# Kernel tuning notes

Measured on AMD Instinct MI355X. Metric: run time of the kernel, lower is better.

## Reference

```python
import jax, jax.numpy as jnp
import numpy as np

N, E = 50000, 800000          # nodes, directed edges
DIN, DH, DOUT = 128, 256, 128  # feature dims


def setup_inputs() -> dict:
    key = jax.random.key(0)
    ks = jax.random.split(key, 8)
    glorot = lambda k, fin, fout: jax.random.normal(k, (fin, fout), jnp.float32) * np.float32(1.0 / np.sqrt(fin))
    x = jax.random.normal(ks[0], (N, DIN), jnp.float32)
    edge_index = jax.random.randint(ks[1], (2, E), 0, N, dtype=jnp.int64)
    return {
        "x": x,
        "edge_index": edge_index,
        "W1_l": glorot(ks[2], DIN, DH),   # applied to aggregated neighbors
        "b1": jnp.zeros((DH,), jnp.float32),
        "W1_r": glorot(ks[3], DIN, DH),   # root weight
        "W2_l": glorot(ks[4], DH, DOUT),
        "b2": jnp.zeros((DOUT,), jnp.float32),
        "W2_r": glorot(ks[5], DH, DOUT),
    }


def _sage_conv(x, src, dst, W_l, b, W_r):
    """PyG SAGEConv (mean aggr): lin_l(mean_j x_j) + lin_r(x_i)."""
    n = x.shape[0]
    agg = jax.ops.segment_sum(x[src], dst, num_segments=n)          # [N, D]
    deg = jax.ops.segment_sum(jnp.ones((src.shape[0], 1), x.dtype), dst, num_segments=n)
    agg = agg / jnp.maximum(deg, 1.0)                               # mean over in-neighbors
    return agg @ W_l + b + x @ W_r


def reference(x, edge_index, W1_l, b1, W1_r, W2_l, b2, W2_r):
    src, dst = edge_index[0], edge_index[1]
    h = jax.nn.relu(_sage_conv(x, src, dst, W1_l, b1, W1_r))
    return _sage_conv(h, src, dst, W2_l, b2, W2_r)
```

## Files before the change

### kernel.cpp

```cpp
#include <hip/hip_runtime.h>
#include <hip/hip_bf16.h>
#include <cstdint>


static inline size_t align_up(size_t x, size_t a) { return (x + a - 1) & ~(a - 1); }

using short8 = __attribute__((ext_vector_type(8))) short;
using f32x4  = __attribute__((ext_vector_type(4))) float;

#define BSHIFT 6
#define PB 98

__device__ __forceinline__ float bfpair_lo(unsigned int v) {
  union { unsigned int i; float f; } u; u.i = v << 16; return u.f;
}
__device__ __forceinline__ float bfpair_hi(unsigned int v) {
  union { unsigned int i; float f; } u; u.i = v & 0xffff0000u; return u.f;
}
__device__ __forceinline__ unsigned short f2bf(float f) {
  union { float f; unsigned int i; } u; u.f = f;
  unsigned int r = u.i + 0x7fffu + ((u.i >> 16) & 1u);
  return (unsigned short)(r >> 16);
}

__device__ __forceinline__ void gload_lds16(const void* g, void* l) {
  __builtin_amdgcn_global_load_lds(
      (const __attribute__((address_space(1))) void*)g,
      (__attribute__((address_space(3))) void*)l, 16, 0, 0);
}


__global__ __launch_bounds__(256) void bhist_kernel(const int* __restrict__ dst,
                                                    int* __restrict__ blockhist,
                                                    int E, int chunk) {
  __shared__ int h[1024];
  const int t = threadIdx.x;
  const int pb = blockIdx.x;
  #pragma unroll
  for (int i = t; i < 1024; i += 256) h[i] = 0;
  __syncthreads();
  const int e0 = pb * chunk;
  int e1 = e0 + chunk; if (e1 > E) e1 = E;
  for (int e = e0 + t; e < e1; e += 256) atomicAdd(&h[dst[e] >> BSHIFT], 1);
  __syncthreads();
  #pragma unroll
  for (int i = t; i < 1024; i += 256) blockhist[pb * 1024 + i] = h[i];
}

__global__ __launch_bounds__(256) void colscan_kernel(int* __restrict__ blockhist,
                                                      int* __restrict__ bhist) {
  const int i = blockIdx.x * 256 + threadIdx.x;
  int run = 0;
  #pragma unroll 7
  for (int pb = 0; pb < PB; ++pb) {
    int v = blockhist[pb * 1024 + i];
    blockhist[pb * 1024 + i] = run;
    run += v;
  }
  bhist[i] = run;
}

__global__ __launch_bounds__(256) void bscan_kernel(const int* __restrict__ bhist,
                                                    int* __restrict__ brow, int NB) {
  const int t = threadIdx.x;
  int4 v = *reinterpret_cast<const int4*>(bhist + t * 4);
  int tsum = v.x + v.y + v.z + v.w;
  const int lane = t & 63, w = t >> 6;
  int inc = tsum;
  #pragma unroll
  for (int off = 1; off < 64; off <<= 1) {
    int u = __shfl_up(inc, off, 64);
    if (lane >= off) inc += u;
  }
  __shared__ int wsum[4];
  if (lane == 63) wsum[w] = inc;
  __syncthreads();
  int woff = 0;
  for (int i = 0; i < w; ++i) woff += wsum[i];
  int e0 = woff + inc - tsum;
  const int base = t * 4;
  int p[4];
  p[0] = e0;
  p[1] = e0 + v.x;
  p[2] = p[1] + v.y;
  p[3] = p[2] + v.z;
  #pragma unroll
  for (int j = 0; j < 4; ++j)
    if (base + j < NB) brow[base + j] = p[j];
  if (t == 0) brow[NB] = wsum[0] + wsum[1] + wsum[2] + wsum[3];
}

__global__ __launch_bounds__(256) void bin2_kernel(const int* __restrict__ src,
                                                   const int* __restrict__ dst,
                                                   const int* __restrict__ brow,
                                                   const int* __restrict__ blockhist,
                                                   unsigned* __restrict__ stage,
                                                   int E, int NB, int chunk) {
  __shared__ int cur[1024];
  const int t = threadIdx.x;
  const int pb = blockIdx.x;
  for (int i = t; i < 1024; i += 256)
    cur[i] = (i < NB) ? (brow[i] + blockhist[pb * 1024 + i]) : 0;
  __syncthreads();
  const int e0 = pb * chunk;
  int e1 = e0 + chunk; if (e1 > E) e1 = E;
  for (int e = e0 + t; e < e1; e += 256) {
    int d = dst[e];
    int p = atomicAdd(&cur[d >> BSHIFT], 1);
    stage[p] = (unsigned)src[e] | ((unsigned)(d & 63) << 16);
  }
}

__global__ __launch_bounds__(256) void scatter2b_kernel(const unsigned* __restrict__ stage,
                                                        const int* __restrict__ brow,
                                                        int* __restrict__ rowptr,
                                                        unsigned short* __restrict__ col,
                                                        int N, int E) {
  __shared__ int dcnt[64];
  __shared__ int dbase[64];
  const int b = blockIdx.x;
  const int t = threadIdx.x;
  const int n0 = b << BSHIFT;
  const int lo = brow[b], hi = brow[b + 1];
  if (t < 64) dcnt[t] = 0;
  __syncthreads();
  for (int e = lo + t; e < hi; e += 256) atomicAdd(&dcnt[stage[e] >> 16], 1);
  __syncthreads();
  if (t < 64) {
    int v = dcnt[t];
    int inc = v;
    #pragma unroll
    for (int off = 1; off < 64; off <<= 1) {
      int u = __shfl_up(inc, off, 64);
      if (t >= off) inc += u;
    }
    int excl = lo + inc - v;
    dbase[t] = excl;
    dcnt[t] = 0;
    if (n0 + t < N) rowptr[n0 + t] = excl;
  }
  if (b == 0 && t == 0) rowptr[N] = E;
  __syncthreads();
  for (int e = lo + t; e < hi; e += 256) {
    unsigned pr = stage[e];
    int d = pr >> 16;
    int p = atomicAdd(&dcnt[d], 1);
    col[dbase[d] + p] = (unsigned short)(pr & 0xffffu);
  }
}

__global__ void build_bt_kernel(const float* __restrict__ W1l, const float* __restrict__ W1r,
                                const float* __restrict__ W2l, const float* __restrict__ W2r,
                                __hip_bfloat16* __restrict__ BT1,
                                __hip_bfloat16* __restrict__ BT2) {
  int bb = blockIdx.x;
  int idx = (bb & 255) * 256 + threadIdx.x;
  int n = idx >> 8, k = idx & 255;
  if (bb < 256) {
    float v = (k < 128) ? W1l[k * 256 + n] : W1r[(k - 128) * 256 + n];
    BT1[idx] = __float2bfloat16(v);
  } else {
    float v = (n < 128) ? W2l[k * 128 + n] : W2r[k * 128 + (n - 128)];
    BT2[idx] = __float2bfloat16(v);
  }
}

__global__ void convert_x_kernel(const float* __restrict__ x, __hip_bfloat16* __restrict__ A1,
                                 int total4) {
  int idx = blockIdx.x * blockDim.x + threadIdx.x;
  if (idx >= total4) return;
  int i = idx >> 5, j4 = (idx & 31) << 2;
  float4 v = *reinterpret_cast<const float4*>(x + (size_t)i * 128 + j4);
  unsigned int p0 = ((unsigned)f2bf(v.y) << 16) | f2bf(v.x);
  unsigned int p1 = ((unsigned)f2bf(v.w) << 16) | f2bf(v.z);
  uint2 pk = make_uint2(p0, p1);
  *reinterpret_cast<uint2*>(A1 + (size_t)i * 256 + 128 + j4) = pk;
}


__global__ __launch_bounds__(64) void agg1_kernel(const int* __restrict__ rowptr,
                                                  const unsigned short* __restrict__ col,
                                                  __hip_bfloat16* __restrict__ A1) {
  const int i = blockIdx.x;
  const int t = threadIdx.x;
  const int beg = rowptr[i], end = rowptr[i + 1];
  float ax = 0.f, ay = 0.f;
  int e = beg;
  for (; e + 3 < end; e += 4) {
    int s0 = col[e], s1 = col[e + 1], s2 = col[e + 2], s3 = col[e + 3];
    unsigned v0 = *reinterpret_cast<const unsigned*>(A1 + (size_t)s0 * 256 + 128 + t * 2);
    unsigned v1 = *reinterpret_cast<const unsigned*>(A1 + (size_t)s1 * 256 + 128 + t * 2);
    unsigned v2 = *reinterpret_cast<const unsigned*>(A1 + (size_t)s2 * 256 + 128 + t * 2);
    unsigned v3 = *reinterpret_cast<const unsigned*>(A1 + (size_t)s3 * 256 + 128 + t * 2);
    ax += (bfpair_lo(v0) + bfpair_lo(v1)) + (bfpair_lo(v2) + bfpair_lo(v3));
    ay += (bfpair_hi(v0) + bfpair_hi(v1)) + (bfpair_hi(v2) + bfpair_hi(v3));
  }
  for (; e < end; ++e) {
    int s0 = col[e];
    unsigned v0 = *reinterpret_cast<const unsigned*>(A1 + (size_t)s0 * 256 + 128 + t * 2);
    ax += bfpair_lo(v0);
    ay += bfpair_hi(v0);
  }
  int d = end - beg;
  float inv = 1.0f / (float)(d > 1 ? d : 1);
  unsigned pk = ((unsigned)f2bf(ay * inv) << 16) | f2bf(ax * inv);
  *reinterpret_cast<unsigned*>(A1 + (size_t)i * 256 + t * 2) = pk;
}

__global__ __launch_bounds__(64) void agg2_kernel(const __hip_bfloat16* __restrict__ hw2,
                                                  const int* __restrict__ rowptr,
                                                  const unsigned short* __restrict__ col,
                                                  const float* __restrict__ b2,
                                                  float* __restrict__ out) {
  const int i = blockIdx.x;
  const int t = threadIdx.x;
  const int beg = rowptr[i], end = rowptr[i + 1];
  float ax = 0.f, ay = 0.f;
  int e = beg;
  for (; e + 3 < end; e += 4) {
    int s0 = col[e], s1 = col[e + 1], s2 = col[e + 2], s3 = col[e + 3];
    unsigned v0 = *reinterpret_cast<const unsigned*>(hw2 + (size_t)s0 * 256 + t * 2);
    unsigned v1 = *reinterpret_cast<const unsigned*>(hw2 + (size_t)s1 * 256 + t * 2);
    unsigned v2 = *reinterpret_cast<const unsigned*>(hw2 + (size_t)s2 * 256 + t * 2);
    unsigned v3 = *reinterpret_cast<const unsigned*>(hw2 + (size_t)s3 * 256 + t * 2);
    ax += (bfpair_lo(v0) + bfpair_lo(v1)) + (bfpair_lo(v2) + bfpair_lo(v3));
    ay += (bfpair_hi(v0) + bfpair_hi(v1)) + (bfpair_hi(v2) + bfpair_hi(v3));
  }
  for (; e < end; ++e) {
    int s0 = col[e];
    unsigned v0 = *reinterpret_cast<const unsigned*>(hw2 + (size_t)s0 * 256 + t * 2);
    ax += bfpair_lo(v0);
    ay += bfpair_hi(v0);
  }
  int d = end - beg;
  float inv = 1.0f / (float)(d > 1 ? d : 1);
  unsigned sv = *reinterpret_cast<const unsigned*>(hw2 + (size_t)i * 256 + 128 + t * 2);
  float2 bb = *reinterpret_cast<const float2*>(b2 + t * 2);
  float2 r;
  r.x = ax * inv + bfpair_lo(sv) + bb.x;
  r.y = ay * inv + bfpair_hi(sv) + bb.y;
  *reinterpret_cast<float2*>(out + (size_t)i * 128 + t * 2) = r;
}

template <bool BIAS_RELU>
__global__ __launch_bounds__(256) void mfma_gemm_kernel(
    const __hip_bfloat16* __restrict__ A,
    const __hip_bfloat16* __restrict__ BT,
    const float* __restrict__ bias,
    __hip_bfloat16* __restrict__ C,
    int M) {
  __shared__ __hip_bfloat16 As[128 * 32];
  __shared__ __hip_bfloat16 Bs[128 * 32];
  const int t = threadIdx.x;
  const int lane = t & 63;
  const int w = t >> 6;
  const int bm = blockIdx.x * 128;
  const int bn = blockIdx.y * 128;
  const int wr = (w >> 1) * 64;
  const int wc = (w & 1) * 64;

  const int srow = lane >> 2;
  const int sbyte = (lane & 3) * 16;

  f32x4 acc[4][4];
  #pragma unroll
  for (int i = 0; i < 4; ++i)
    #pragma unroll
    for (int j = 0; j < 4; ++j) acc[i][j] = (f32x4)(0.f);

  const int frow_a = wr + (lane & 15);
  const int frow_b = wc + (lane & 15);
  const int fbyte = (lane >> 4) * 16;

  for (int k0 = 0; k0 < 256; k0 += 32) {
    #pragma unroll
    for (int q = 0; q < 2; ++q) {
      const int chunk = w * 2 + q;
      const int row = chunk * 16 + srow;
      int gr = bm + row;
      if (gr >= M) gr = M - 1;
      gload_lds16((const char*)A + (size_t)gr * 512 + k0 * 2 + sbyte,
                  (char*)As + chunk * 1024);
      gload_lds16((const char*)BT + (size_t)(bn + row) * 512 + k0 * 2 + sbyte,
                  (char*)Bs + chunk * 1024);
    }
    __syncthreads();
    short8 af[4], bf[4];
    #pragma unroll
    for (int i = 0; i < 4; ++i) {
      af[i] = *reinterpret_cast<const short8*>((const char*)As + (frow_a + i * 16) * 64 + fbyte);
      bf[i] = *reinterpret_cast<const short8*>((const char*)Bs + (frow_b + i * 16) * 64 + fbyte);
    }
    #pragma unroll
    for (int i = 0; i < 4; ++i)
      #pragma unroll
      for (int j = 0; j < 4; ++j)
        acc[i][j] = __builtin_amdgcn_mfma_f32_16x16x32_bf16(af[i], bf[j], acc[i][j], 0, 0, 0);
    __syncthreads();
  }

  const int crow0 = bm + wr + (lane >> 4) * 4;
  const int ccol0 = bn + wc + (lane & 15);
  float bj[4] = {0.f, 0.f, 0.f, 0.f};
  if (BIAS_RELU) {
    #pragma unroll
    for (int j = 0; j < 4; ++j) bj[j] = bias[ccol0 + j * 16];
  }
  #pragma unroll
  for (int i = 0; i < 4; ++i) {
    #pragma unroll
    for (int q = 0; q < 4; ++q) {
      const int r = crow0 + i * 16 + q;
      if (r < M) {
        #pragma unroll
        for (int j = 0; j < 4; ++j) {
          float v = acc[i][j][q];
          if (BIAS_RELU) v = fmaxf(v + bj[j], 0.f);
          C[(size_t)r * 256 + ccol0 + j * 16] = __float2bfloat16(v);
        }
      }
    }
  }
}


extern "C" void kernel_launch(void* const* d_in, const int* in_sizes, int n_in,
                              void* d_out, int out_size, void* d_ws, size_t ws_size,
                              hipStream_t stream) {
  const float* x    = (const float*)d_in[0];
  const int*   edge = (const int*)d_in[1];
  const float* W1_l = (const float*)d_in[2];
  const float* b1   = (const float*)d_in[3];
  const float* W1_r = (const float*)d_in[4];
  const float* W2_l = (const float*)d_in[5];
  const float* b2   = (const float*)d_in[6];
  const float* W2_r = (const float*)d_in[7];
  float* out = (float*)d_out;

  const int N = in_sizes[0] / 128;
  const int E = in_sizes[1] / 2;
  const int* srcv = edge;
  const int* dstv = edge + E;
  const int NB = (N + (1 << BSHIFT) - 1) >> BSHIFT;

  char* ws = (char*)d_ws;
  size_t off = 0;
  auto alloc = [&](size_t bytes) -> void* {
    void* p = ws + off;
    off += align_up(bytes, 256);
    return p;
  };
  int* rowptr    = (int*)alloc((size_t)(N + 1) * 4);
  int* brow      = (int*)alloc((size_t)(NB + 1) * 4);
  int* bhist     = (int*)alloc(1024 * 4);
  int* blockhist = (int*)alloc((size_t)PB * 1024 * 4);
  unsigned short* col = (unsigned short*)alloc((size_t)E * 2);
  unsigned* stage = (unsigned*)alloc((size_t)E * 4);
  __hip_bfloat16* BT1 = (__hip_bfloat16*)alloc(256 * 256 * 2);
  __hip_bfloat16* BT2 = (__hip_bfloat16*)alloc(256 * 256 * 2);
  __hip_bfloat16* A1  = (__hip_bfloat16*)alloc((size_t)N * 256 * 2);
  __hip_bfloat16* h   = (__hip_bfloat16*)alloc((size_t)N * 256 * 2);
  __hip_bfloat16* hw2 = (__hip_bfloat16*)alloc((size_t)N * 256 * 2);

  build_bt_kernel<<<512, 256, 0, stream>>>(W1_l, W1_r, W2_l, W2_r, BT1, BT2);
  convert_x_kernel<<<(N * 32 + 255) / 256, 256, 0, stream>>>(x, A1, N * 32);

  const int chunk = (E + PB - 1) / PB;
  bhist_kernel<<<PB, 256, 0, stream>>>(dstv, blockhist, E, chunk);
  colscan_kernel<<<4, 256, 0, stream>>>(blockhist, bhist);
  bscan_kernel<<<1, 256, 0, stream>>>(bhist, brow, NB);
  bin2_kernel<<<PB, 256, 0, stream>>>(srcv, dstv, brow, blockhist, stage, E, NB, chunk);
  scatter2b_kernel<<<NB, 256, 0, stream>>>(stage, brow, rowptr, col, N, E);

  agg1_kernel<<<N, 64, 0, stream>>>(rowptr, col, A1);

  dim3 gemm_grid((N + 127) / 128, 2);
  mfma_gemm_kernel<true><<<gemm_grid, 256, 0, stream>>>(A1, BT1, b1, h, N);
  mfma_gemm_kernel<false><<<gemm_grid, 256, 0, stream>>>(h, BT2, nullptr, hw2, N);

  agg2_kernel<<<N, 64, 0, stream>>>(hw2, rowptr, col, b2, out);
}
```

Before: 165.1 us.

## Fuse both GEMMs via LDS-resident hidden tile and merge prep and scan kernels

```diff
diff --git a/kernel.cpp b/kernel.cpp
--- a/kernel.cpp
+++ b/kernel.cpp
@@ -47,47 +47,30 @@
   for (int i = t; i < 1024; i += 256) blockhist[pb * 1024 + i] = h[i];
 }
 
-__global__ __launch_bounds__(256) void colscan_kernel(int* __restrict__ blockhist,
-                                                      int* __restrict__ bhist) {
-  const int i = blockIdx.x * 256 + threadIdx.x;
+__global__ __launch_bounds__(1024) void scan_all_kernel(int* __restrict__ blockhist,
+                                                        int* __restrict__ brow, int NB) {
+  const int i = threadIdx.x;
   int run = 0;
-  #pragma unroll 7
   for (int pb = 0; pb < PB; ++pb) {
     int v = blockhist[pb * 1024 + i];
     blockhist[pb * 1024 + i] = run;
     run += v;
   }
-  bhist[i] = run;
-}
-
-__global__ __launch_bounds__(256) void bscan_kernel(const int* __restrict__ bhist,
-                                                    int* __restrict__ brow, int NB) {
-  const int t = threadIdx.x;
-  int4 v = *reinterpret_cast<const int4*>(bhist + t * 4);
-  int tsum = v.x + v.y + v.z + v.w;
-  const int lane = t & 63, w = t >> 6;
-  int inc = tsum;
+  const int lane = i & 63, w = i >> 6;
+  int inc = run;
   #pragma unroll
   for (int off = 1; off < 64; off <<= 1) {
     int u = __shfl_up(inc, off, 64);
     if (lane >= off) inc += u;
   }
-  __shared__ int wsum[4];
+  __shared__ int wsum[16];
   if (lane == 63) wsum[w] = inc;
   __syncthreads();
   int woff = 0;
-  for (int i = 0; i < w; ++i) woff += wsum[i];
-  int e0 = woff + inc - tsum;
-  const int base = t * 4;
-  int p[4];
-  p[0] = e0;
-  p[1] = e0 + v.x;
-  p[2] = p[1] + v.y;
-  p[3] = p[2] + v.z;
-  #pragma unroll
-  for (int j = 0; j < 4; ++j)
-    if (base + j < NB) brow[base + j] = p[j];
-  if (t == 0) brow[NB] = wsum[0] + wsum[1] + wsum[2] + wsum[3];
+  for (int k = 0; k < w; ++k) woff += wsum[k];
+  int excl = woff + inc - run;
+  if (i < NB) brow[i] = excl;
+  if (i == 1023) brow[NB] = woff + inc;
 }
 
 __global__ __launch_bounds__(256) void bin2_kernel(const int* __restrict__ src,
@@ -149,32 +132,33 @@
   }
 }
 
-__global__ void build_bt_kernel(const float* __restrict__ W1l, const float* __restrict__ W1r,
-                                const float* __restrict__ W2l, const float* __restrict__ W2r,
-                                __hip_bfloat16* __restrict__ BT1,
-                                __hip_bfloat16* __restrict__ BT2) {
-  int bb = blockIdx.x;
-  int idx = (bb & 255) * 256 + threadIdx.x;
-  int n = idx >> 8, k = idx & 255;
-  if (bb < 256) {
-    float v = (k < 128) ? W1l[k * 256 + n] : W1r[(k - 128) * 256 + n];
-    BT1[idx] = __float2bfloat16(v);
-  } else {
-    float v = (n < 128) ? W2l[k * 128 + n] : W2r[k * 128 + (n - 128)];
-    BT2[idx] = __float2bfloat16(v);
-  }
-}
-
-__global__ void convert_x_kernel(const float* __restrict__ x, __hip_bfloat16* __restrict__ A1,
-                                 int total4) {
-  int idx = blockIdx.x * blockDim.x + threadIdx.x;
+__global__ __launch_bounds__(256) void prep_kernel(
+    const float* __restrict__ x,
+    const float* __restrict__ W1l, const float* __restrict__ W1r,
+    const float* __restrict__ W2l, const float* __restrict__ W2r,
+    __hip_bfloat16* __restrict__ BT1, __hip_bfloat16* __restrict__ BT2,
+    __hip_bfloat16* __restrict__ A1, int total4) {
+  const int bb = blockIdx.x;
+  const int t = threadIdx.x;
+  if (bb < 512) {
+    int idx = (bb & 255) * 256 + t;
+    int n = idx >> 8, k = idx & 255;
+    if (bb < 256) {
+      float v = (k < 128) ? W1l[k * 256 + n] : W1r[(k - 128) * 256 + n];
+      BT1[idx] = __float2bfloat16(v);
+    } else {
+      float v = (n < 128) ? W2l[k * 128 + n] : W2r[k * 128 + (n - 128)];
+      BT2[idx] = __float2bfloat16(v);
+    }
+    return;
+  }
+  int idx = (bb - 512) * 256 + t;
   if (idx >= total4) return;
   int i = idx >> 5, j4 = (idx & 31) << 2;
   float4 v = *reinterpret_cast<const float4*>(x + (size_t)i * 128 + j4);
-  unsigned int p0 = ((unsigned)f2bf(v.y) << 16) | f2bf(v.x);
-  unsigned int p1 = ((unsigned)f2bf(v.w) << 16) | f2bf(v.z);
-  uint2 pk = make_uint2(p0, p1);
-  *reinterpret_cast<uint2*>(A1 + (size_t)i * 256 + 128 + j4) = pk;
+  unsigned p0 = ((unsigned)f2bf(v.y) << 16) | f2bf(v.x);
+  unsigned p1 = ((unsigned)f2bf(v.w) << 16) | f2bf(v.z);
+  *reinterpret_cast<uint2*>(A1 + (size_t)i * 256 + 128 + j4) = make_uint2(p0, p1);
 }
 
 
@@ -242,25 +226,27 @@
   *reinterpret_cast<float2*>(out + (size_t)i * 128 + t * 2) = r;
 }
 
-template <bool BIAS_RELU>
-__global__ __launch_bounds__(256) void mfma_gemm_kernel(
-    const __hip_bfloat16* __restrict__ A,
-    const __hip_bfloat16* __restrict__ BT,
-    const float* __restrict__ bias,
-    __hip_bfloat16* __restrict__ C,
+__global__ __launch_bounds__(256) void gemm_fused_kernel(
+    const __hip_bfloat16* __restrict__ A1,
+    const __hip_bfloat16* __restrict__ BT1,
+    const __hip_bfloat16* __restrict__ BT2,
+    const float* __restrict__ b1,
+    __hip_bfloat16* __restrict__ hw2,
     int M) {
-  __shared__ __hip_bfloat16 As[128 * 32];
-  __shared__ __hip_bfloat16 Bs[128 * 32];
+  __shared__ __hip_bfloat16 As[64 * 32];
+  __shared__ __hip_bfloat16 Bs[256 * 32];
+  __shared__ __hip_bfloat16 hLds[64 * 256];
   const int t = threadIdx.x;
   const int lane = t & 63;
   const int w = t >> 6;
-  const int bm = blockIdx.x * 128;
-  const int bn = blockIdx.y * 128;
-  const int wr = (w >> 1) * 64;
-  const int wc = (w & 1) * 64;
-
-  const int srow = lane >> 2;
+  const int wc = w * 64;
+  const int bm = blockIdx.x * 64;
+
+  const int srow4 = lane >> 2;
   const int sbyte = (lane & 3) * 16;
+  const int fr = lane & 15;
+  const int fbyte = (lane >> 4) * 16;
+  const int kslot = lane >> 4;
 
   f32x4 acc[4][4];
   #pragma unroll
@@ -268,28 +254,26 @@
     #pragma unroll
     for (int j = 0; j < 4; ++j) acc[i][j] = (f32x4)(0.f);
 
-  const int frow_a = wr + (lane & 15);
-  const int frow_b = wc + (lane & 15);
-  const int fbyte = (lane >> 4) * 16;
-
   for (int k0 = 0; k0 < 256; k0 += 32) {
-    #pragma unroll
-    for (int q = 0; q < 2; ++q) {
-      const int chunk = w * 2 + q;
-      const int row = chunk * 16 + srow;
-      int gr = bm + row;
+    {
+      int gr = bm + w * 16 + srow4;
       if (gr >= M) gr = M - 1;
-      gload_lds16((const char*)A + (size_t)gr * 512 + k0 * 2 + sbyte,
-                  (char*)As + chunk * 1024);
-      gload_lds16((const char*)BT + (size_t)(bn + row) * 512 + k0 * 2 + sbyte,
-                  (char*)Bs + chunk * 1024);
+      gload_lds16((const char*)A1 + (size_t)gr * 512 + k0 * 2 + sbyte,
+                  (char*)As + w * 1024);
+    }
+    #pragma unroll
+    for (int q = 0; q < 4; ++q) {
+      const int c = w * 4 + q;
+      const int row = c * 16 + srow4;
+      gload_lds16((const char*)BT1 + (size_t)row * 512 + k0 * 2 + sbyte,
+                  (char*)Bs + c * 1024);
     }
     __syncthreads();
     short8 af[4], bf[4];
     #pragma unroll
     for (int i = 0; i < 4; ++i) {
-      af[i] = *reinterpret_cast<const short8*>((const char*)As + (frow_a + i * 16) * 64 + fbyte);
-      bf[i] = *reinterpret_cast<const short8*>((const char*)Bs + (frow_b + i * 16) * 64 + fbyte);
+      af[i] = *reinterpret_cast<const short8*>((const char*)As + (fr + i * 16) * 64 + fbyte);
+      bf[i] = *reinterpret_cast<const short8*>((const char*)Bs + (wc + fr + i * 16) * 64 + fbyte);
     }
     #pragma unroll
     for (int i = 0; i < 4; ++i)
@@ -299,24 +283,71 @@
     __syncthreads();
   }
 
-  const int crow0 = bm + wr + (lane >> 4) * 4;
-  const int ccol0 = bn + wc + (lane & 15);
-  float bj[4] = {0.f, 0.f, 0.f, 0.f};
-  if (BIAS_RELU) {
-    #pragma unroll
-    for (int j = 0; j < 4; ++j) bj[j] = bias[ccol0 + j * 16];
-  }
+  {
+    const int c0 = wc + fr;
+    const int r0 = (lane >> 4) * 4;
+    float bj[4];
+    #pragma unroll
+    for (int j = 0; j < 4; ++j) bj[j] = b1[c0 + j * 16];
+    #pragma unroll
+    for (int i = 0; i < 4; ++i) {
+      #pragma unroll
+      for (int j = 0; j < 4; ++j) {
+        const int c = c0 + j * 16;
+        #pragma unroll
+        for (int q = 0; q < 4; ++q) {
+          const int r = r0 + i * 16 + q;
+          float v = fmaxf(acc[i][j][q] + bj[j], 0.f);
+          const int byte = r * 512 + (((c >> 3) ^ (r & 7)) << 4) + ((c & 7) << 1);
+          *reinterpret_cast<__hip_bfloat16*>((char*)hLds + byte) = __float2bfloat16(v);
+        }
+      }
+    }
+  }
+
   #pragma unroll
-  for (int i = 0; i < 4; ++i) {
+  for (int i = 0; i < 4; ++i)
+    #pragma unroll
+    for (int j = 0; j < 4; ++j) acc[i][j] = (f32x4)(0.f);
+
+  for (int k0 = 0; k0 < 256; k0 += 32) {
     #pragma unroll
     for (int q = 0; q < 4; ++q) {
-      const int r = crow0 + i * 16 + q;
-      if (r < M) {
-        #pragma unroll
-        for (int j = 0; j < 4; ++j) {
-          float v = acc[i][j][q];
-          if (BIAS_RELU) v = fmaxf(v + bj[j], 0.f);
-          C[(size_t)r * 256 + ccol0 + j * 16] = __float2bfloat16(v);
+      const int c = w * 4 + q;
+      const int row = c * 16 + srow4;
+      gload_lds16((const char*)BT2 + (size_t)row * 512 + k0 * 2 + sbyte,
+                  (char*)Bs + c * 1024);
+    }
+    __syncthreads();
+    short8 af[4], bf[4];
+    const int ks = (k0 >> 3) + kslot;
+    #pragma unroll
+    for (int i = 0; i < 4; ++i) {
+      const int ra = fr + i * 16;
+      af[i] = *reinterpret_cast<const short8*>(
+          (const char*)hLds + ra * 512 + ((ks ^ (ra & 7)) << 4));
+      bf[i] = *reinterpret_cast<const short8*>((const char*)Bs + (wc + fr + i * 16) * 64 + fbyte);
+    }
+    #pragma unroll
+    for (int i = 0; i < 4; ++i)
+      #pragma unroll
+      for (int j = 0; j < 4; ++j)
+        acc[i][j] = __builtin_amdgcn_mfma_f32_16x16x32_bf16(af[i], bf[j], acc[i][j], 0, 0, 0);
+    __syncthreads();
+  }
+
+  {
+    const int c0 = wc + fr;
+    const int r0 = (lane >> 4) * 4;
+    #pragma unroll
+    for (int i = 0; i < 4; ++i) {
+      #pragma unroll
+      for (int q = 0; q < 4; ++q) {
+        const int r = bm + r0 + i * 16 + q;
+        if (r < M) {
+          #pragma unroll
+          for (int j = 0; j < 4; ++j)
+            hw2[(size_t)r * 256 + c0 + j * 16] = __float2bfloat16(acc[i][j][q]);
         }
       }
     }
@@ -352,31 +383,27 @@
   };
   int* rowptr    = (int*)alloc((size_t)(N + 1) * 4);
   int* brow      = (int*)alloc((size_t)(NB + 1) * 4);
-  int* bhist     = (int*)alloc(1024 * 4);
   int* blockhist = (int*)alloc((size_t)PB * 1024 * 4);
   unsigned short* col = (unsigned short*)alloc((size_t)E * 2);
   unsigned* stage = (unsigned*)alloc((size_t)E * 4);
   __hip_bfloat16* BT1 = (__hip_bfloat16*)alloc(256 * 256 * 2);
   __hip_bfloat16* BT2 = (__hip_bfloat16*)alloc(256 * 256 * 2);
   __hip_bfloat16* A1  = (__hip_bfloat16*)alloc((size_t)N * 256 * 2);
-  __hip_bfloat16* h   = (__hip_bfloat16*)alloc((size_t)N * 256 * 2);
   __hip_bfloat16* hw2 = (__hip_bfloat16*)alloc((size_t)N * 256 * 2);
 
-  build_bt_kernel<<<512, 256, 0, stream>>>(W1_l, W1_r, W2_l, W2_r, BT1, BT2);
-  convert_x_kernel<<<(N * 32 + 255) / 256, 256, 0, stream>>>(x, A1, N * 32);
+  const int conv_blocks = (N * 32 + 255) / 256;
+  prep_kernel<<<512 + conv_blocks, 256, 0, stream>>>(x, W1_l, W1_r, W2_l, W2_r,
+                                                     BT1, BT2, A1, N * 32);
 
   const int chunk = (E + PB - 1) / PB;
   bhist_kernel<<<PB, 256, 0, stream>>>(dstv, blockhist, E, chunk);
-  colscan_kernel<<<4, 256, 0, stream>>>(blockhist, bhist);
-  bscan_kernel<<<1, 256, 0, stream>>>(bhist, brow, NB);
+  scan_all_kernel<<<1, 1024, 0, stream>>>(blockhist, brow, NB);
   bin2_kernel<<<PB, 256, 0, stream>>>(srcv, dstv, brow, blockhist, stage, E, NB, chunk);
   scatter2b_kernel<<<NB, 256, 0, stream>>>(stage, brow, rowptr, col, N, E);
 
   agg1_kernel<<<N, 64, 0, stream>>>(rowptr, col, A1);
 
-  dim3 gemm_grid((N + 127) / 128, 2);
-  mfma_gemm_kernel<true><<<gemm_grid, 256, 0, stream>>>(A1, BT1, b1, h, N);
-  mfma_gemm_kernel<false><<<gemm_grid, 256, 0, stream>>>(h, BT2, nullptr, hw2, N);
+  gemm_fused_kernel<<<(N + 63) / 64, 256, 0, stream>>>(A1, BT1, BT2, b1, hw2, N);
 
   agg2_kernel<<<N, 64, 0, stream>>>(hw2, rowptr, col, b2, out);
 }
```

Result: faster. 159.6 us (-3.3%).
